# Optimization experiments

Hardware: AMD Instinct MI355X
Metric: run time of the kernel (lower is better)

The kernel has to match this reference:

```python
import jax, jax.numpy as jnp
import numpy as np

B, L, D = 2, 2048, 1024
H = 16
HD = D // H  # 64


def _orthogonal_projection(key, d, m):
    g = jax.random.normal(key, (d, m), dtype=jnp.float32)
    q, r = jnp.linalg.qr(g)
    s = jnp.sign(jnp.diagonal(r))
    s = jnp.where(s == 0, 1.0, s)
    q = q * s[None, :]
    # preserve_variance=True
    return q * np.sqrt(d / m)


def setup_inputs() -> dict:
    key = jax.random.key(0)
    ks = jax.random.split(key, 8)
    x = jax.random.normal(ks[0], (B, L, D), dtype=jnp.float32)
    p = jax.random.normal(ks[1], (B, L, D), dtype=jnp.float32)
    s = 1.0 / np.sqrt(D)
    W_qkv = jax.random.uniform(ks[2], (3 * D, D), dtype=jnp.float32, minval=-s, maxval=s)
    b_qkv = jax.random.uniform(ks[3], (3 * D,), dtype=jnp.float32, minval=-s, maxval=s)
    W_out = jax.random.uniform(ks[4], (D, D), dtype=jnp.float32, minval=-s, maxval=s)
    b_out = jax.random.uniform(ks[5], (D,), dtype=jnp.float32, minval=-s, maxval=s)
    proj = _orthogonal_projection(ks[6], D, D // 2)
    return {"x": x, "p": p, "W_qkv": W_qkv, "b_qkv": b_qkv,
            "W_out": W_out, "b_out": b_out, "proj": proj}


def reference(x, p, W_qkv, b_qkv, W_out, b_out, proj):
    # QKV projection: (B,L,D) -> (B,L,3,H,HD)
    qkv = (jnp.einsum('bld,ed->ble', x, W_qkv) + b_qkv).reshape(B, L, 3, H, HD)
    q, k, v = qkv[:, :, 0], qkv[:, :, 1], qkv[:, :, 2]

    # Collaborative rotary phases from conditioning tokens: (B,L,H,HD/2)
    phases = (p @ proj).reshape(B, L, H, HD // 2)  # phase_scale = 1.0
    cos, sin = jnp.cos(phases), jnp.sin(phases)

    half = HD // 2
    # non-interleaved rotary: split head_dim into two halves
    def rot(t):
        t1, t2 = t[..., :half], t[..., half:]
        return jnp.concatenate([t1 * cos - t2 * sin, t1 * sin + t2 * cos], axis=-1)

    q, k = rot(q), rot(k)

    scale = HD ** -0.5
    scores = jnp.einsum('bqhd,bkhd->bhqk', q, k) * scale
    attn = jax.nn.softmax(scores, axis=-1)
    out = jnp.einsum('bhqk,bkhd->bqhd', attn, v).reshape(B, L, D)
    return jnp.einsum('bld,ed->ble', out, W_out) + b_out
```

## Files before the change

### kernel.cpp

```cpp
#include <hip/hip_runtime.h>
#include <hip/hip_bf16.h>
#include <math.h>

namespace {
constexpr int Bb = 2;
constexpr int Ll = 2048;
constexpr int Dd = 1024;
constexpr int Hh = 16;
constexpr int NT = Bb * Ll;
constexpr int D3 = 3 * Dd;
constexpr int PH = Dd / 2;
}

typedef __attribute__((ext_vector_type(8))) short bf16x8;
typedef __attribute__((ext_vector_type(4))) float f32x4;

__device__ inline unsigned pack2bf(float a, float b) {
  __hip_bfloat162 t = __float22bfloat162_rn(float2{a, b});
  union { __hip_bfloat162 h; unsigned u; } cv; cv.h = t;
  return cv.u;
}

__device__ inline float bfhalf(unsigned u, int hi) {
  union { unsigned u; float f; } c;
  c.u = hi ? (u & 0xffff0000u) : (u << 16);
  return c.f;
}

__device__ inline void async_cp16(const void* gsrc, void* ldst) {
  __builtin_amdgcn_global_load_lds(
      (const __attribute__((address_space(1))) unsigned int*)gsrc,
      (__attribute__((address_space(3))) unsigned int*)ldst, 16, 0, 0);
}

__global__ __launch_bounds__(256) void prep_kernel(
    const float4* __restrict__ p, uint2* __restrict__ p_hi4, uint2* __restrict__ p_lo4,
    const float* __restrict__ proj, short* __restrict__ th, short* __restrict__ tl,
    const float4* __restrict__ x, const float4* __restrict__ wq, const float4* __restrict__ wo,
    uint2* __restrict__ xd, uint2* __restrict__ wqd, uint2* __restrict__ wod)
{
  __shared__ float Ls[64][65];
  const int bid = blockIdx.x;
  const int tid = threadIdx.x;

  if (bid < 4096) {
    const int i = bid * 256 + tid;
    const float4 f = p[i];
    float hf[4], lf[4];
    const float ff[4] = {f.x, f.y, f.z, f.w};
#pragma unroll
    for (int j = 0; j < 4; ++j) {
      const __hip_bfloat16 h = __float2bfloat16(ff[j]);
      hf[j] = __bfloat162float(h);
      lf[j] = ff[j] - hf[j];
    }
    p_hi4[i] = make_uint2(pack2bf(hf[0], hf[1]), pack2bf(hf[2], hf[3]));
    p_lo4[i] = make_uint2(pack2bf(lf[0], lf[1]), pack2bf(lf[2], lf[3]));
  } else if (bid < 4224) {
    const int bx = bid - 4096;
    const int d0 = (bx & 15) * 64, m0 = (bx >> 4) * 64;
    const int r = tid >> 4, c4 = (tid & 15) * 4;
#pragma unroll
    for (int it = 0; it < 4; ++it) {
      const int row = it * 16 + r;
      const float4 v = *(const float4*)&proj[(size_t)(d0 + row) * PH + m0 + c4];
      Ls[row][c4] = v.x; Ls[row][c4+1] = v.y; Ls[row][c4+2] = v.z; Ls[row][c4+3] = v.w;
    }
    __syncthreads();
#pragma unroll
    for (int it = 0; it < 4; ++it) {
      const int row = it * 16 + r;
      float hf[4], lf[4];
#pragma unroll
      for (int j = 0; j < 4; ++j) {
        const float v = Ls[c4 + j][row];
        const __hip_bfloat16 h = __float2bfloat16(v);
        hf[j] = __bfloat162float(h);
        lf[j] = v - hf[j];
      }
      *(uint2*)&th[(size_t)(m0 + row) * Dd + d0 + c4] = make_uint2(pack2bf(hf[0], hf[1]), pack2bf(hf[2], hf[3]));
      *(uint2*)&tl[(size_t)(m0 + row) * Dd + d0 + c4] = make_uint2(pack2bf(lf[0], lf[1]), pack2bf(lf[2], lf[3]));
    }
  } else {
    int i = (bid - 4224) * 256 + tid;
    const float4* s; uint2* d;
    if (i < 1048576) { s = x; d = xd; }
    else if (i < 1048576 + 786432) { i -= 1048576; s = wq; d = wqd; }
    else { i -= 1048576 + 786432; s = wo; d = wod; }
    const float4 f = s[i];
    d[i] = make_uint2(pack2bf(f.x, f.y), pack2bf(f.z, f.w));
  }
}

__global__ __launch_bounds__(256) void gemm_nn_split(
    const short* __restrict__ Ah_g, const short* __restrict__ Al_g,
    const short* __restrict__ Wh_g, const short* __restrict__ Wl_g,
    float* __restrict__ C)
{
  __shared__ __align__(16) short Ah[64 * 32], Al[64 * 32], Wh[64 * 32], Wl[64 * 32];
  const int tid = threadIdx.x;
  const int w = tid >> 6, lane = tid & 63;
  const int l15 = lane & 15, quad = lane >> 4;
  const int n0 = blockIdx.y * 64, m0 = blockIdx.x * 64;

  const int row = tid >> 2, cc = tid & 3;
  const int ksw = (cc ^ (row & 3)) * 8;
  const short* gAh = Ah_g + (size_t)(n0 + row) * Dd + ksw;
  const short* gAl = Al_g + (size_t)(n0 + row) * Dd + ksw;
  const short* gWh = Wh_g + (size_t)(m0 + row) * Dd + ksw;
  const short* gWl = Wl_g + (size_t)(m0 + row) * Dd + ksw;
  short* lAh = Ah + tid * 8;
  short* lAl = Al + tid * 8;
  short* lWh = Wh + tid * 8;
  short* lWl = Wl + tid * 8;

  f32x4 acc[4];
#pragma unroll
  for (int j = 0; j < 4; ++j) acc[j] = f32x4{0.f, 0.f, 0.f, 0.f};

  const int swq = (quad ^ (l15 & 3)) * 8;

  for (int k0 = 0; k0 < Dd; k0 += 32) {
    __syncthreads();
    async_cp16(gAh + k0, lAh);
    async_cp16(gAl + k0, lAl);
    async_cp16(gWh + k0, lWh);
    async_cp16(gWl + k0, lWl);
    __syncthreads();

    bf16x8 ah, al, wh[4], wl[4];
    ah = *(const bf16x8*)&Ah[(w * 16 + l15) * 32 + swq];
    al = *(const bf16x8*)&Al[(w * 16 + l15) * 32 + swq];
#pragma unroll
    for (int j = 0; j < 4; ++j) {
      wh[j] = *(const bf16x8*)&Wh[(j * 16 + l15) * 32 + swq];
      wl[j] = *(const bf16x8*)&Wl[(j * 16 + l15) * 32 + swq];
    }
#pragma unroll
    for (int j = 0; j < 4; ++j) {
      acc[j] = __builtin_amdgcn_mfma_f32_16x16x32_bf16(ah, wh[j], acc[j], 0, 0, 0);
      acc[j] = __builtin_amdgcn_mfma_f32_16x16x32_bf16(ah, wl[j], acc[j], 0, 0, 0);
      acc[j] = __builtin_amdgcn_mfma_f32_16x16x32_bf16(al, wh[j], acc[j], 0, 0, 0);
    }
  }

#pragma unroll
  for (int r = 0; r < 4; ++r) {
    float* crow = C + (size_t)(n0 + w * 16 + quad * 4 + r) * PH + m0 + l15;
#pragma unroll
    for (int j = 0; j < 4; ++j) crow[j * 16] = acc[j][r];
  }
}

__global__ __launch_bounds__(256) void gemm_qkv_fused(
    const __hip_bfloat16* __restrict__ A, const __hip_bfloat16* __restrict__ W,
    const float* __restrict__ bias, const float* __restrict__ phases,
    __hip_bfloat16* __restrict__ q_bf, __hip_bfloat16* __restrict__ k_bf,
    __hip_bfloat16* __restrict__ vt_g)
{
  __shared__ __align__(16) short As[128 * 32];
  __shared__ __align__(16) short Ws[128 * 32];
  const int tid = threadIdx.x;
  const int w = tid >> 6, lane = tid & 63;
  const int l15 = lane & 15, quad = lane >> 4;
  const int wn = w >> 1, wm = w & 1;
  const int n0 = blockIdx.y * 128, m0 = blockIdx.x * 128;

  const int row = tid >> 2, cc = tid & 3;
  const int ksw = (cc ^ (row & 3)) * 8;
  const short* gA  = (const short*)A + (size_t)(n0 + row) * Dd + ksw;
  const short* gW  = (const short*)W + (size_t)(m0 + row) * Dd + ksw;
  short* lA  = As + tid * 8;
  short* lA2 = As + 2048 + tid * 8;
  short* lW  = Ws + tid * 8;
  short* lW2 = Ws + 2048 + tid * 8;

  f32x4 acc[4][4];
#pragma unroll
  for (int i = 0; i < 4; ++i)
#pragma unroll
    for (int j = 0; j < 4; ++j) acc[i][j] = f32x4{0.f, 0.f, 0.f, 0.f};

  const int swq = (quad ^ (l15 & 3)) * 8;

  for (int k0 = 0; k0 < Dd; k0 += 32) {
    __syncthreads();
    async_cp16(gA + k0, lA);
    async_cp16(gA + 64 * Dd + k0, lA2);
    async_cp16(gW + k0, lW);
    async_cp16(gW + 64 * Dd + k0, lW2);
    __syncthreads();

    bf16x8 af[4], bf[4];
#pragma unroll
    for (int i = 0; i < 4; ++i)
      af[i] = *(const bf16x8*)&As[(wn * 64 + i * 16 + l15) * 32 + swq];
#pragma unroll
    for (int j = 0; j < 4; ++j)
      bf[j] = *(const bf16x8*)&Ws[(wm * 64 + j * 16 + l15) * 32 + swq];
#pragma unroll
    for (int i = 0; i < 4; ++i)
#pragma unroll
      for (int j = 0; j < 4; ++j)
        acc[i][j] = __builtin_amdgcn_mfma_f32_16x16x32_bf16(af[i], bf[j], acc[i][j], 0, 0, 0);
  }

  float bv[4];
#pragma unroll
  for (int j = 0; j < 4; ++j) bv[j] = bias[m0 + wm * 64 + j * 16 + l15];

  const int region = m0 >> 10;
  const int mloc = (m0 & 1023) + wm * 64;
  const int h = mloc >> 6;

  if (region < 2) {
    __hip_bfloat16* dst = region == 0 ? q_bf : k_bf;
    const float SC = region == 0 ? 0.18033688011112042f : 1.0f;
    const int dosw = (region == 1);
#pragma unroll
    for (int i = 0; i < 4; ++i)
#pragma unroll
      for (int r = 0; r < 4; ++r) {
        const int n = n0 + wn * 64 + i * 16 + quad * 4 + r;
        const int swz = dosw ? (((quad * 4 + r) & 7) << 3) : 0;
        const float* phrow = phases + (size_t)n * PH + h * 32;
        __hip_bfloat16* drow = dst + (size_t)n * Dd + h * 64;
#pragma unroll
        for (int pz = 0; pz < 2; ++pz) {
          const float ph = phrow[pz * 16 + l15];
          float sn, cs;
          __sincosf(ph, &sn, &cs);
          const float a1 = acc[i][pz][r] + bv[pz];
          const float a2 = acc[i][pz + 2][r] + bv[pz + 2];
          drow[(pz * 16 + l15) ^ swz]      = __float2bfloat16((a1 * cs - a2 * sn) * SC);
          drow[(pz * 16 + 32 + l15) ^ swz] = __float2bfloat16((a1 * sn + a2 * cs) * SC);
        }
      }
  } else {
    const int bh = (n0 >> 11) * 16 + h;
    const int tokb = (n0 & 2047) + wn * 64;
    const int vsw = (l15 & 7) << 3;
#pragma unroll
    for (int i = 0; i < 4; ++i)
#pragma unroll
      for (int j = 0; j < 4; ++j) {
        const uint2 o = make_uint2(
            pack2bf(acc[i][j][0] + bv[j], acc[i][j][1] + bv[j]),
            pack2bf(acc[i][j][2] + bv[j], acc[i][j][3] + bv[j]));
        const int d = j * 16 + l15;
        *(uint2*)&vt_g[(size_t)(bh * 64 + d) * Ll + tokb + ((i * 16 + quad * 4) ^ vsw)] = o;
      }
  }
}

__global__ __launch_bounds__(256) void gemm_bt_64(
    const __hip_bfloat16* __restrict__ A, const __hip_bfloat16* __restrict__ W,
    const float* __restrict__ bias, float* __restrict__ C, int K, int M)
{
  __shared__ __align__(16) short As[128 * 32];
  __shared__ __align__(16) short Ws[64 * 32];
  const int tid = threadIdx.x;
  const int w = tid >> 6, lane = tid & 63;
  const int l15 = lane & 15, quad = lane >> 4;
  const int n0 = blockIdx.y * 128, m0 = blockIdx.x * 64;

  const int row = tid >> 2, cc = tid & 3;
  const int ksw = (cc ^ (row & 3)) * 8;
  const short* gA = (const short*)A + (size_t)(n0 + row) * K + ksw;
  const short* gW = (const short*)W + (size_t)(m0 + row) * K + ksw;
  short* lA  = As + tid * 8;
  short* lA2 = As + 2048 + tid * 8;
  short* lW  = Ws + tid * 8;

  f32x4 acc[2][4];
#pragma unroll
  for (int i = 0; i < 2; ++i)
#pragma unroll
    for (int j = 0; j < 4; ++j) acc[i][j] = f32x4{0.f, 0.f, 0.f, 0.f};

  const int swq = (quad ^ (l15 & 3)) * 8;

  for (int k0 = 0; k0 < K; k0 += 32) {
    __syncthreads();
    async_cp16(gA + k0, lA);
    async_cp16(gA + 64 * K + k0, lA2);
    async_cp16(gW + k0, lW);
    __syncthreads();

    bf16x8 af[2], bf[4];
#pragma unroll
    for (int i = 0; i < 2; ++i)
      af[i] = *(const bf16x8*)&As[(w * 32 + i * 16 + l15) * 32 + swq];
#pragma unroll
    for (int j = 0; j < 4; ++j)
      bf[j] = *(const bf16x8*)&Ws[(j * 16 + l15) * 32 + swq];
#pragma unroll
    for (int i = 0; i < 2; ++i)
#pragma unroll
      for (int j = 0; j < 4; ++j)
        acc[i][j] = __builtin_amdgcn_mfma_f32_16x16x32_bf16(af[i], bf[j], acc[i][j], 0, 0, 0);
  }

  float bv[4];
#pragma unroll
  for (int j = 0; j < 4; ++j) bv[j] = bias[m0 + j * 16 + l15];
#pragma unroll
  for (int i = 0; i < 2; ++i)
#pragma unroll
    for (int r = 0; r < 4; ++r) {
      float* crow = C + (size_t)(n0 + w * 32 + i * 16 + quad * 4 + r) * M + m0 + l15;
#pragma unroll
      for (int j = 0; j < 4; ++j) crow[j * 16] = acc[i][j][r] + bv[j];
    }
}

__global__ __launch_bounds__(256) void attn_mfma(
    const __hip_bfloat16* __restrict__ q_bf,
    const __hip_bfloat16* __restrict__ k_bf,
    const __hip_bfloat16* __restrict__ vt_g,
    __hip_bfloat16* __restrict__ o_part,
    float* __restrict__ lden_g)
{
  __shared__ __align__(16) short KV[2][2][4096];

  const int tid = threadIdx.x;
  const int w = tid >> 6;
  const int lane = tid & 63;
  const int l15 = lane & 15;
  const int quad = lane >> 4;

  const int q0 = blockIdx.x * 128;
  const int bh = blockIdx.y;
  const int kz = blockIdx.z;
  const int b = bh >> 4, h = bh & 15;
  const int kt0 = kz * 16;

  bf16x8 qfrag[2][2];
#pragma unroll
  for (int qg = 0; qg < 2; ++qg)
#pragma unroll
    for (int kh = 0; kh < 2; ++kh) {
      const size_t qrow = (size_t)(b * Ll + q0 + w * 32 + qg * 16 + l15);
      qfrag[qg][kh] = *(const bf16x8*)(q_bf + qrow * Dd + h * 64 + kh * 32 + quad * 8);
    }

  f32x4 acc[4][2];
#pragma unroll
  for (int dt = 0; dt < 4; ++dt)
#pragma unroll
    for (int qg = 0; qg < 2; ++qg) acc[dt][qg] = f32x4{0.f, 0.f, 0.f, 0.f};
  f32x4 lden[2] = {f32x4{0.f,0.f,0.f,0.f}, f32x4{0.f,0.f,0.f,0.f}};
  const short one_bf = (short)0x3F80;
  const bf16x8 ones8 = {one_bf, one_bf, one_bf, one_bf, one_bf, one_bf, one_bf, one_bf};

  const __hip_bfloat16* ksrc = k_bf + ((size_t)(b * Ll) + (tid >> 3)) * Dd + h * 64 + (tid & 7) * 8;
  const __hip_bfloat16* vsrc = vt_g + ((size_t)(bh * 64) + (tid >> 3)) * Ll + (tid & 7) * 8;
  const int ldst = tid * 8;

  const int sw = (l15 & 7) << 3;
  const int co0 = (quad * 8) ^ sw;
  const int co1 = (32 + quad * 8) ^ sw;

  {
    const __hip_bfloat16* kp = ksrc + (size_t)kt0 * 64 * Dd;
    const __hip_bfloat16* vp = vsrc + (size_t)kt0 * 64;
    async_cp16(kp,                    &KV[0][0][ldst]);
    async_cp16(kp + (size_t)32 * Dd,  &KV[0][0][2048 + ldst]);
    async_cp16(vp,                    &KV[0][1][ldst]);
    async_cp16(vp + (size_t)32 * Ll,  &KV[0][1][2048 + ldst]);
  }

  for (int kt = 0; kt < 16; ++kt) {
    __syncthreads();
    const int cur = kt & 1;
    if (kt + 1 < 16) {
      const int ktn = kt0 + kt + 1;
      const __hip_bfloat16* kp = ksrc + (size_t)ktn * 64 * Dd;
      const __hip_bfloat16* vp = vsrc + (size_t)ktn * 64;
      async_cp16(kp,                    &KV[cur ^ 1][0][ldst]);
      async_cp16(kp + (size_t)32 * Dd,  &KV[cur ^ 1][0][2048 + ldst]);
      async_cp16(vp,                    &KV[cur ^ 1][1][ldst]);
      async_cp16(vp + (size_t)32 * Ll,  &KV[cur ^ 1][1][2048 + ldst]);
    }
    const short* Ks = &KV[cur][0][0];
    const short* Vt = &KV[cur][1][0];

    f32x4 s[4][2];
#pragma unroll
    for (int n = 0; n < 4; ++n)
#pragma unroll
      for (int qg = 0; qg < 2; ++qg) s[n][qg] = f32x4{0.f, 0.f, 0.f, 0.f};

    __builtin_amdgcn_s_setprio(1);
#pragma unroll
    for (int n = 0; n < 4; ++n) {
      const bf16x8 af0 = *(const bf16x8*)&Ks[(n * 16 + l15) * 64 + co0];
      const bf16x8 af1 = *(const bf16x8*)&Ks[(n * 16 + l15) * 64 + co1];
      s[n][0] = __builtin_amdgcn_mfma_f32_16x16x32_bf16(af0, qfrag[0][0], s[n][0], 0, 0, 0);
      s[n][1] = __builtin_amdgcn_mfma_f32_16x16x32_bf16(af0, qfrag[1][0], s[n][1], 0, 0, 0);
      s[n][0] = __builtin_amdgcn_mfma_f32_16x16x32_bf16(af1, qfrag[0][1], s[n][0], 0, 0, 0);
      s[n][1] = __builtin_amdgcn_mfma_f32_16x16x32_bf16(af1, qfrag[1][1], s[n][1], 0, 0, 0);
    }
    __builtin_amdgcn_s_setprio(0);

    uint2 bq[4][2];
#pragma unroll
    for (int qg = 0; qg < 2; ++qg)
#pragma unroll
      for (int n = 0; n < 4; ++n) {
        union { float f; unsigned u; } p0, p1, p2, p3;
        p0.f = __builtin_amdgcn_exp2f(s[n][qg][0]);
        p1.f = __builtin_amdgcn_exp2f(s[n][qg][1]);
        p2.f = __builtin_amdgcn_exp2f(s[n][qg][2]);
        p3.f = __builtin_amdgcn_exp2f(s[n][qg][3]);
        bq[n][qg] = make_uint2(__builtin_amdgcn_perm(p1.u, p0.u, 0x07060302u),
                               __builtin_amdgcn_perm(p3.u, p2.u, 0x07060302u));
      }

#pragma unroll
    for (int pr = 0; pr < 2; ++pr) {
      const int cop = pr ? co1 : co0;
      bf16x8 va[4];
#pragma unroll
      for (int dt = 0; dt < 4; ++dt)
        va[dt] = *(const bf16x8*)&Vt[(dt * 16 + l15) * 64 + cop];
#pragma unroll
      for (int qg = 0; qg < 2; ++qg) {
        const uint2 a = bq[2 * pr][qg];
        const uint2 c = bq[2 * pr + 1][qg];
        auto rx32 = __builtin_amdgcn_permlane32_swap(a.x, c.x, false, false);
        auto rx16 = __builtin_amdgcn_permlane16_swap(rx32[0], rx32[1], false, false);
        auto ry32 = __builtin_amdgcn_permlane32_swap(a.y, c.y, false, false);
        auto ry16 = __builtin_amdgcn_permlane16_swap(ry32[0], ry32[1], false, false);
        union { unsigned u[4]; bf16x8 v; } pb;
        pb.u[0] = rx16[0]; pb.u[1] = ry16[0]; pb.u[2] = rx16[1]; pb.u[3] = ry16[1];
        __builtin_amdgcn_s_setprio(1);
        lden[qg] = __builtin_amdgcn_mfma_f32_16x16x32_bf16(ones8, pb.v, lden[qg], 0, 0, 0);
#pragma unroll
        for (int dt = 0; dt < 4; ++dt)
          acc[dt][qg] = __builtin_amdgcn_mfma_f32_16x16x32_bf16(va[dt], pb.v, acc[dt][qg], 0, 0, 0);
        __builtin_amdgcn_s_setprio(0);
      }
    }
  }

#pragma unroll
  for (int qg = 0; qg < 2; ++qg) {
    const float lv = lden[qg][0];
    const float linv = 1.f / lv;
    const int ql = q0 + w * 32 + qg * 16 + l15;
    if (quad == 0)
      lden_g[((size_t)(kz * Bb + b) * Hh + h) * Ll + ql] = lv;
    __hip_bfloat16* dst = o_part + ((size_t)kz * NT + b * Ll + ql) * Dd + h * 64;
#pragma unroll
    for (int dt = 0; dt < 4; ++dt) {
      const uint2 o = make_uint2(
          pack2bf(acc[dt][qg][0] * linv, acc[dt][qg][1] * linv),
          pack2bf(acc[dt][qg][2] * linv, acc[dt][qg][3] * linv));
      *(uint2*)&dst[dt * 16 + quad * 4] = o;
    }
  }
}

__global__ __launch_bounds__(256) void attn_combine(
    const __hip_bfloat16* __restrict__ o_part, const float* __restrict__ lden_g,
    __hip_bfloat16* __restrict__ aout)
{
  const int i = blockIdx.x * 256 + threadIdx.x;
  const int n = i >> 8, d4 = i & 255;
  const int b = n >> 11, l = n & 2047;
  const int h = d4 >> 4;
  const float l0 = lden_g[((size_t)b * Hh + h) * Ll + l];
  const float l1 = lden_g[((size_t)(Bb + b) * Hh + h) * Ll + l];
  const float inv = 1.f / (l0 + l1);
  const float w0 = l0 * inv, w1 = l1 * inv;
  const uint2 a0 = ((const uint2*)o_part)[i];
  const uint2 a1 = ((const uint2*)o_part)[(NT * (size_t)Dd / 4) + i];
  const float r0 = w0 * bfhalf(a0.x, 0) + w1 * bfhalf(a1.x, 0);
  const float r1 = w0 * bfhalf(a0.x, 1) + w1 * bfhalf(a1.x, 1);
  const float r2 = w0 * bfhalf(a0.y, 0) + w1 * bfhalf(a1.y, 0);
  const float r3 = w0 * bfhalf(a0.y, 1) + w1 * bfhalf(a1.y, 1);
  ((uint2*)aout)[i] = make_uint2(pack2bf(r0, r1), pack2bf(r2, r3));
}

extern "C" void kernel_launch(void* const* d_in, const int* in_sizes, int n_in,
                              void* d_out, int out_size, void* d_ws, size_t ws_size,
                              hipStream_t stream) {
  const float* x     = (const float*)d_in[0];
  const float* p     = (const float*)d_in[1];
  const float* W_qkv = (const float*)d_in[2];
  const float* b_qkv = (const float*)d_in[3];
  const float* W_out = (const float*)d_in[4];
  const float* b_out = (const float*)d_in[5];
  const float* proj  = (const float*)d_in[6];
  float* out = (float*)d_out;

  char* wsb = (char*)d_ws;
  float*          phases   = (float*)(wsb);
  short*          p_hi     = (short*)(wsb + (8u << 20));
  __hip_bfloat16* aout_bf  = (__hip_bfloat16*)(wsb + (8u << 20));
  short*          p_lo     = (short*)(wsb + (16u << 20));
  __hip_bfloat16* vt_g     = (__hip_bfloat16*)(wsb + (16u << 20));
  short*          projt_hi = (short*)(wsb + (24u << 20));
  short*          projt_lo = (short*)(wsb + (25u << 20));
  __hip_bfloat16* q_bf     = (__hip_bfloat16*)(wsb + (26u << 20));
  __hip_bfloat16* k_bf     = (__hip_bfloat16*)(wsb + (34u << 20));
  __hip_bfloat16* x_bf     = (__hip_bfloat16*)(wsb + (42u << 20));
  __hip_bfloat16* o_part   = (__hip_bfloat16*)(wsb + (42u << 20));
  __hip_bfloat16* wqkv_bf  = (__hip_bfloat16*)(wsb + (50u << 20));
  __hip_bfloat16* wout_bf  = (__hip_bfloat16*)(wsb + (58u << 20));
  float*          lden_g   = (float*)(wsb + (60u << 20));

  prep_kernel<<<12416, 256, 0, stream>>>(
      (const float4*)p, (uint2*)p_hi, (uint2*)p_lo,
      proj, projt_hi, projt_lo,
      (const float4*)x, (const float4*)W_qkv, (const float4*)W_out,
      (uint2*)x_bf, (uint2*)wqkv_bf, (uint2*)wout_bf);
  gemm_nn_split<<<dim3(PH / 64, NT / 64), 256, 0, stream>>>(p_hi, p_lo, projt_hi, projt_lo, phases);
  gemm_qkv_fused<<<dim3(D3 / 128, NT / 128), 256, 0, stream>>>(x_bf, wqkv_bf, b_qkv, phases,
                                                               q_bf, k_bf, vt_g);
  attn_mfma<<<dim3(Ll / 128, Bb * Hh, 2), 256, 0, stream>>>(q_bf, k_bf, vt_g, o_part, lden_g);
  attn_combine<<<4096, 256, 0, stream>>>(o_part, lden_g, aout_bf);
  gemm_bt_64<<<dim3(Dd / 64, NT / 128), 256, 0, stream>>>(aout_bf, wout_bf, b_out, out, Dd, Dd);
}
```

Measured before the change: 251.3 us.

## Software-pipeline attention loop so next tile's QK overlaps current exp and PV

Splits the K/V shared buffers and restructures the attention inner loop so the QK^T MFMAs for tile i+1 are interleaved with the exp/pack and PV MFMAs for tile i. K is prefetched two tiles ahead and V one tile ahead. The aim is to hide exp (transcendental) latency and the dependency between scores and PV behind independent matrix work. The scores are now carried across iterations, which raises register pressure, and correctness depends on the tricky buffer indexing and async-copy/barrier ordering.

```diff
diff --git a/kernel.cpp b/kernel.cpp
--- a/kernel.cpp
+++ b/kernel.cpp
@@ -321,7 +321,8 @@
     __hip_bfloat16* __restrict__ o_part,
     float* __restrict__ lden_g)
 {
-  __shared__ __align__(16) short KV[2][2][4096];
+  __shared__ __align__(16) short Kb[2][4096];
+  __shared__ __align__(16) short Vb[2][4096];
 
   const int tid = threadIdx.x;
   const int w = tid >> 6;
@@ -350,6 +351,7 @@
 #pragma unroll
     for (int qg = 0; qg < 2; ++qg) acc[dt][qg] = f32x4{0.f, 0.f, 0.f, 0.f};
   f32x4 lden[2] = {f32x4{0.f,0.f,0.f,0.f}, f32x4{0.f,0.f,0.f,0.f}};
+  const f32x4 zro = {0.f, 0.f, 0.f, 0.f};
   const short one_bf = (short)0x3F80;
   const bf16x8 ones8 = {one_bf, one_bf, one_bf, one_bf, one_bf, one_bf, one_bf, one_bf};
 
@@ -361,88 +363,100 @@
   const int co0 = (quad * 8) ^ sw;
   const int co1 = (32 + quad * 8) ^ sw;
 
-  {
-    const __hip_bfloat16* kp = ksrc + (size_t)kt0 * 64 * Dd;
-    const __hip_bfloat16* vp = vsrc + (size_t)kt0 * 64;
-    async_cp16(kp,                    &KV[0][0][ldst]);
-    async_cp16(kp + (size_t)32 * Dd,  &KV[0][0][2048 + ldst]);
-    async_cp16(vp,                    &KV[0][1][ldst]);
-    async_cp16(vp + (size_t)32 * Ll,  &KV[0][1][2048 + ldst]);
-  }
-
-  for (int kt = 0; kt < 16; ++kt) {
-    __syncthreads();
-    const int cur = kt & 1;
-    if (kt + 1 < 16) {
-      const int ktn = kt0 + kt + 1;
-      const __hip_bfloat16* kp = ksrc + (size_t)ktn * 64 * Dd;
-      const __hip_bfloat16* vp = vsrc + (size_t)ktn * 64;
-      async_cp16(kp,                    &KV[cur ^ 1][0][ldst]);
-      async_cp16(kp + (size_t)32 * Dd,  &KV[cur ^ 1][0][2048 + ldst]);
-      async_cp16(vp,                    &KV[cur ^ 1][1][ldst]);
-      async_cp16(vp + (size_t)32 * Ll,  &KV[cur ^ 1][1][2048 + ldst]);
-    }
-    const short* Ks = &KV[cur][0][0];
-    const short* Vt = &KV[cur][1][0];
-
-    f32x4 s[4][2];
-#pragma unroll
-    for (int n = 0; n < 4; ++n)
-#pragma unroll
-      for (int qg = 0; qg < 2; ++qg) s[n][qg] = f32x4{0.f, 0.f, 0.f, 0.f};
-
-    __builtin_amdgcn_s_setprio(1);
-#pragma unroll
-    for (int n = 0; n < 4; ++n) {
-      const bf16x8 af0 = *(const bf16x8*)&Ks[(n * 16 + l15) * 64 + co0];
-      const bf16x8 af1 = *(const bf16x8*)&Ks[(n * 16 + l15) * 64 + co1];
-      s[n][0] = __builtin_amdgcn_mfma_f32_16x16x32_bf16(af0, qfrag[0][0], s[n][0], 0, 0, 0);
-      s[n][1] = __builtin_amdgcn_mfma_f32_16x16x32_bf16(af0, qfrag[1][0], s[n][1], 0, 0, 0);
-      s[n][0] = __builtin_amdgcn_mfma_f32_16x16x32_bf16(af1, qfrag[0][1], s[n][0], 0, 0, 0);
-      s[n][1] = __builtin_amdgcn_mfma_f32_16x16x32_bf16(af1, qfrag[1][1], s[n][1], 0, 0, 0);
-    }
-    __builtin_amdgcn_s_setprio(0);
-
-    uint2 bq[4][2];
-#pragma unroll
-    for (int qg = 0; qg < 2; ++qg)
-#pragma unroll
-      for (int n = 0; n < 4; ++n) {
-        union { float f; unsigned u; } p0, p1, p2, p3;
-        p0.f = __builtin_amdgcn_exp2f(s[n][qg][0]);
-        p1.f = __builtin_amdgcn_exp2f(s[n][qg][1]);
-        p2.f = __builtin_amdgcn_exp2f(s[n][qg][2]);
-        p3.f = __builtin_amdgcn_exp2f(s[n][qg][3]);
-        bq[n][qg] = make_uint2(__builtin_amdgcn_perm(p1.u, p0.u, 0x07060302u),
-                               __builtin_amdgcn_perm(p3.u, p2.u, 0x07060302u));
-      }
-
-#pragma unroll
-    for (int pr = 0; pr < 2; ++pr) {
-      const int cop = pr ? co1 : co0;
+#define STAGE_K(t, bf) { const __hip_bfloat16* kp_ = ksrc + (size_t)(t) * 64 * Dd; \
+  async_cp16(kp_, &Kb[bf][ldst]); async_cp16(kp_ + (size_t)32 * Dd, &Kb[bf][2048 + ldst]); }
+#define STAGE_V(t, bf) { const __hip_bfloat16* vp_ = vsrc + (size_t)(t) * 64; \
+  async_cp16(vp_, &Vb[bf][ldst]); async_cp16(vp_ + (size_t)32 * Ll, &Vb[bf][2048 + ldst]); }
+
+  f32x4 s[4][2];
+
+#define QK_N(Ks, n) { \
+  const bf16x8 af0_ = *(const bf16x8*)&(Ks)[((n) * 16 + l15) * 64 + co0]; \
+  const bf16x8 af1_ = *(const bf16x8*)&(Ks)[((n) * 16 + l15) * 64 + co1]; \
+  s[n][0] = __builtin_amdgcn_mfma_f32_16x16x32_bf16(af0_, qfrag[0][0], zro, 0, 0, 0); \
+  s[n][1] = __builtin_amdgcn_mfma_f32_16x16x32_bf16(af0_, qfrag[1][0], zro, 0, 0, 0); \
+  s[n][0] = __builtin_amdgcn_mfma_f32_16x16x32_bf16(af1_, qfrag[0][1], s[n][0], 0, 0, 0); \
+  s[n][1] = __builtin_amdgcn_mfma_f32_16x16x32_bf16(af1_, qfrag[1][1], s[n][1], 0, 0, 0); }
+
+#define EXPPACK(v, dst) { union { float f; unsigned u; } p0_, p1_, p2_, p3_; \
+  p0_.f = __builtin_amdgcn_exp2f((v)[0]); p1_.f = __builtin_amdgcn_exp2f((v)[1]); \
+  p2_.f = __builtin_amdgcn_exp2f((v)[2]); p3_.f = __builtin_amdgcn_exp2f((v)[3]); \
+  dst = make_uint2(__builtin_amdgcn_perm(p1_.u, p0_.u, 0x07060302u), \
+                   __builtin_amdgcn_perm(p3_.u, p2_.u, 0x07060302u)); }
+
+#define PV_QG(va, aU, cU, qg) { \
+  auto rx32_ = __builtin_amdgcn_permlane32_swap((aU).x, (cU).x, false, false); \
+  auto rx16_ = __builtin_amdgcn_permlane16_swap(rx32_[0], rx32_[1], false, false); \
+  auto ry32_ = __builtin_amdgcn_permlane32_swap((aU).y, (cU).y, false, false); \
+  auto ry16_ = __builtin_amdgcn_permlane16_swap(ry32_[0], ry32_[1], false, false); \
+  union { unsigned u[4]; bf16x8 v; } pb_; \
+  pb_.u[0] = rx16_[0]; pb_.u[1] = ry16_[0]; pb_.u[2] = rx16_[1]; pb_.u[3] = ry16_[1]; \
+  lden[qg] = __builtin_amdgcn_mfma_f32_16x16x32_bf16(ones8, pb_.v, lden[qg], 0, 0, 0); \
+  acc[0][qg] = __builtin_amdgcn_mfma_f32_16x16x32_bf16(va[0], pb_.v, acc[0][qg], 0, 0, 0); \
+  acc[1][qg] = __builtin_amdgcn_mfma_f32_16x16x32_bf16(va[1], pb_.v, acc[1][qg], 0, 0, 0); \
+  acc[2][qg] = __builtin_amdgcn_mfma_f32_16x16x32_bf16(va[2], pb_.v, acc[2][qg], 0, 0, 0); \
+  acc[3][qg] = __builtin_amdgcn_mfma_f32_16x16x32_bf16(va[3], pb_.v, acc[3][qg], 0, 0, 0); }
+
+  STAGE_K(kt0, 0);
+  __syncthreads();
+  STAGE_K(kt0 + 1, 1);
+  STAGE_V(kt0, 0);
+  __builtin_amdgcn_s_setprio(1);
+  QK_N(Kb[0], 0); QK_N(Kb[0], 1); QK_N(Kb[0], 2); QK_N(Kb[0], 3);
+  __builtin_amdgcn_s_setprio(0);
+
+  for (int i = 0; i < 16; ++i) {
+    __syncthreads();
+    if (i + 2 < 16) STAGE_K(kt0 + i + 2, i & 1);
+    if (i + 1 < 16) STAGE_V(kt0 + i + 1, (i + 1) & 1);
+    const short* Kn = &Kb[(i + 1) & 1][0];
+    const short* Vc = &Vb[i & 1][0];
+    const bool doqk = (i + 1 < 16);
+
+    uint2 a0, a1, c0, c1;
+    EXPPACK(s[0][0], a0); EXPPACK(s[0][1], a1);
+    EXPPACK(s[1][0], c0); EXPPACK(s[1][1], c1);
+    if (doqk) {
+      __builtin_amdgcn_s_setprio(1);
+      QK_N(Kn, 0); QK_N(Kn, 1);
+      __builtin_amdgcn_s_setprio(0);
+    }
+    {
       bf16x8 va[4];
 #pragma unroll
       for (int dt = 0; dt < 4; ++dt)
-        va[dt] = *(const bf16x8*)&Vt[(dt * 16 + l15) * 64 + cop];
-#pragma unroll
-      for (int qg = 0; qg < 2; ++qg) {
-        const uint2 a = bq[2 * pr][qg];
-        const uint2 c = bq[2 * pr + 1][qg];
-        auto rx32 = __builtin_amdgcn_permlane32_swap(a.x, c.x, false, false);
-        auto rx16 = __builtin_amdgcn_permlane16_swap(rx32[0], rx32[1], false, false);
-        auto ry32 = __builtin_amdgcn_permlane32_swap(a.y, c.y, false, false);
-        auto ry16 = __builtin_amdgcn_permlane16_swap(ry32[0], ry32[1], false, false);
-        union { unsigned u[4]; bf16x8 v; } pb;
-        pb.u[0] = rx16[0]; pb.u[1] = ry16[0]; pb.u[2] = rx16[1]; pb.u[3] = ry16[1];
-        __builtin_amdgcn_s_setprio(1);
-        lden[qg] = __builtin_amdgcn_mfma_f32_16x16x32_bf16(ones8, pb.v, lden[qg], 0, 0, 0);
-#pragma unroll
-        for (int dt = 0; dt < 4; ++dt)
-          acc[dt][qg] = __builtin_amdgcn_mfma_f32_16x16x32_bf16(va[dt], pb.v, acc[dt][qg], 0, 0, 0);
-        __builtin_amdgcn_s_setprio(0);
-      }
-    }
-  }
+        va[dt] = *(const bf16x8*)&Vc[(dt * 16 + l15) * 64 + co0];
+      __builtin_amdgcn_s_setprio(1);
+      PV_QG(va, a0, c0, 0);
+      PV_QG(va, a1, c1, 1);
+      __builtin_amdgcn_s_setprio(0);
+    }
+
+    uint2 a2, a3, c2, c3;
+    EXPPACK(s[2][0], a2); EXPPACK(s[2][1], a3);
+    EXPPACK(s[3][0], c2); EXPPACK(s[3][1], c3);
+    if (doqk) {
+      __builtin_amdgcn_s_setprio(1);
+      QK_N(Kn, 2); QK_N(Kn, 3);
+      __builtin_amdgcn_s_setprio(0);
+    }
+    {
+      bf16x8 va[4];
+#pragma unroll
+      for (int dt = 0; dt < 4; ++dt)
+        va[dt] = *(const bf16x8*)&Vc[(dt * 16 + l15) * 64 + co1];
+      __builtin_amdgcn_s_setprio(1);
+      PV_QG(va, a2, c2, 0);
+      PV_QG(va, a3, c3, 1);
+      __builtin_amdgcn_s_setprio(0);
+    }
+  }
+
+#undef STAGE_K
+#undef STAGE_V
+#undef QK_N
+#undef EXPPACK
+#undef PV_QG
 
 #pragma unroll
   for (int qg = 0; qg < 2; ++qg) {
```

Result: no change. 249.9 us (-0.6%).
